# Performance work log

Hardware: AMD Instinct MI355X
Metric: run time of the kernel (lower is better)

Reference implementation:

```python
import jax, jax.numpy as jnp
import numpy as np
import math

D_MODEL = 1024
EPS = 1e-6  # RMSNorm epsilon


def setup_inputs() -> dict:
    key = jax.random.key(0)
    ks = jax.random.split(key, 9)
    d = D_MODEL
    B, T = 4, 4096
    s = 1.0 / math.sqrt(d)
    return {
        "x": jax.random.normal(ks[0], (B, T, d), dtype=jnp.float32),
        "w_key": jax.random.normal(ks[1], (2 * d, d), dtype=jnp.float32) * s,  # Linear(d, 2d, bias=False)
        "conv_w": jax.random.normal(ks[2], (d, 1, 3), dtype=jnp.float32) * (1.0 / math.sqrt(3)),  # depthwise k=3
        "conv_b": jax.random.normal(ks[3], (d,), dtype=jnp.float32) * 0.02,
        "w1": jax.random.normal(ks[4], (2 * d, d), dtype=jnp.float32) * s,  # Linear(d, 2d)
        "b1": jax.random.normal(ks[5], (2 * d,), dtype=jnp.float32) * 0.02,
        "w2": jax.random.normal(ks[6], (d, 2 * d), dtype=jnp.float32) * (1.0 / math.sqrt(2 * d)),  # Linear(2d, d)
        "b2": jax.random.normal(ks[7], (d,), dtype=jnp.float32) * 0.02,
        "norm_w": jnp.ones((d,), dtype=jnp.float32),
    }


def parallel_lerp_scan(theta, alpha):
    # h_t = lerp(h_{t-1}, theta_t, alpha_t) = (1-alpha_t)*h_{t-1} + alpha_t*theta_t
    # Linear recurrence h_t = a_t*h_{t-1} + b_t -> log-depth associative scan.
    a = 1.0 - alpha
    b = alpha * theta

    def combine(c1, c2):
        a1, b1 = c1
        a2, b2 = c2
        return (a2 * a1, a2 * b1 + b2)

    _, h = jax.lax.associative_scan(combine, (a, b), axis=1)
    return h


def rms_norm(x, w):
    var = jnp.mean(jnp.square(x), axis=-1, keepdims=True)
    return x * jax.lax.rsqrt(var + EPS) * w


def reference(x, w_key, conv_w, conv_b, w1, b1, w2, b2, norm_w):
    d = x.shape[-1]
    res = jnp.einsum('btd,ed->bte', x, w_key)  # [B,T,2D]
    theta, alpha = res[..., :d], res[..., d:]
    h = parallel_lerp_scan(jnp.tanh(theta) * math.pi, jax.nn.sigmoid(alpha))
    h = h.astype(x.dtype)
    # causal depthwise conv: left-pad (k-1)=2 zeros along time
    h_t = jnp.transpose(h, (0, 2, 1))  # [B,D,T]
    conv = jax.lax.conv_general_dilated(
        h_t, conv_w, window_strides=(1,), padding=[(2, 0)],
        feature_group_count=d, dimension_numbers=('NCH', 'OIH', 'NCH'))
    h_bound = jnp.transpose(conv + conv_b[None, :, None], (0, 2, 1))  # [B,T,D]
    z = h + h_bound
    hid = jax.nn.silu(jnp.einsum('btd,ed->bte', z, w1) + b1)
    h_final = jnp.einsum('bte,de->btd', hid, w2) + b2
    return rms_norm(h_final, norm_w)
```

## Files before the change

### kernel.cpp

```cpp
#include <hip/hip_runtime.h>

typedef unsigned short u16;
typedef unsigned int u32;
typedef __attribute__((ext_vector_type(8))) short short8;
typedef __attribute__((ext_vector_type(4))) float f32x4;

#define T_LEN 4096
#define BATCH 4
#define M_TOT (BATCH*T_LEN)
#define NCHUNK 64
#define CLEN 64

__device__ __forceinline__ u16 f2bf(float f){
  u32 u = __builtin_bit_cast(u32, f);
  u32 r = (u + 0x7FFFu + ((u >> 16) & 1u)) >> 16;
  return (u16)r;
}
__device__ __forceinline__ float bf2f(u16 h){
  u32 u = ((u32)h) << 16; return __builtin_bit_cast(float, u);
}
__device__ __forceinline__ float sigmoid_(float v){ return 1.f/(1.f + __expf(-v)); }
__device__ __forceinline__ float tanh_pi_(float v){
  return 3.14159265358979323846f * (1.f - 2.f/(1.f + __expf(2.f*v)));
}

__global__ __launch_bounds__(256) void cvt_bf16_k(const float* __restrict__ in,
                                                  u16* __restrict__ out, int n4){
  int g = blockIdx.x*256 + threadIdx.x;
  if (g >= n4) return;
  float4 v = reinterpret_cast<const float4*>(in)[g];
  reinterpret_cast<ushort4*>(out)[g] =
      make_ushort4(f2bf(v.x), f2bf(v.y), f2bf(v.z), f2bf(v.w));
}

#define BAR() __builtin_amdgcn_s_barrier()
#define VMCNT(n) asm volatile("s_waitcnt vmcnt(" #n ")" ::: "memory")
#define LGKM0() asm volatile("s_waitcnt lgkmcnt(0)" ::: "memory")
#define LGKM8() asm volatile("s_waitcnt lgkmcnt(8)" ::: "memory")
#define FEN() asm volatile("" ::: "memory")
#define PRIO1() __builtin_amdgcn_s_setprio(1)
#define PRIO0() __builtin_amdgcn_s_setprio(0)

#define STAGE(buf, ab, q, kt) do { \
  const u16* _s = ((ab) ? Bb : Ab) + (size_t)(q)*rowK64 + (size_t)(kt)*64; \
  __builtin_amdgcn_global_load_lds( \
    (const __attribute__((address_space(1))) void*)_s, \
    (__attribute__((address_space(3))) void*)(smem + (buf)*65536 + (ab)*32768 + (q)*8192 + stb), \
    16, 0, 0); \
} while(0)

#define LDA(base, m, kk) (*(const short8*)((base) + (m)*2048 + ((kk) ? csw1 : csw0)))
#define LDB(base, n, kk) (*(const short8*)((base) + (n)*2048 + ((kk) ? csw1 : csw0)))

#define RD_A(base, h) do { _Pragma("unroll") \
  for (int ml=0; ml<4; ml++){ \
    aF[ml*2+0] = LDA(base, 4*(h)+ml, 0); \
    aF[ml*2+1] = LDA(base, 4*(h)+ml, 1); } } while(0)

#define RD_B(base, h) do { _Pragma("unroll") \
  for (int nl=0; nl<2; nl++){ \
    bF[(h)*4+nl*2+0] = LDB(base, 2*(h)+nl, 0); \
    bF[(h)*4+nl*2+1] = LDB(base, 2*(h)+nl, 1); } } while(0)

#define MFMAQ(mh, nh) do { _Pragma("unroll") \
  for (int kk=0; kk<2; kk++) \
  _Pragma("unroll") \
  for (int ml=0; ml<4; ml++) \
  _Pragma("unroll") \
  for (int nl=0; nl<2; nl++) \
    acc[4*(mh)+ml][2*(nh)+nl] = __builtin_amdgcn_mfma_f32_16x16x32_bf16( \
      aF[ml*2+kk], bF[(nh)*4+nl*2+kk], acc[4*(mh)+ml][2*(nh)+nl], 0,0,0); \
} while(0)

template<int EPI>
__global__ __launch_bounds__(512, 2) void gemm8p(
    const u16* __restrict__ Ag, const u16* __restrict__ Bg,
    const float* __restrict__ bias, void* __restrict__ Cout,
    int M, int N, int K)
{
  extern __shared__ __attribute__((aligned(16))) char smem[];
  const int tid = threadIdx.x;
  const int wid = tid >> 6, lane = tid & 63;
  const int wr = wid >> 2, wc = wid & 3;
  const int fr = lane & 15, fq = lane >> 4;

  const int nbn = N >> 8;
  const int nwg = gridDim.x;
  const int bid = blockIdx.x;
  const int swzb = (bid & 7) * (nwg >> 3) + (bid >> 3);
  const int bm = swzb / nbn, bn = swzb - bm * nbn;

  const size_t rowK64 = (size_t)64 * K;
  const u16* Ab = Ag + ((size_t)bm*256 + (tid>>3)) * K + ((tid & 7) ^ ((tid >> 3) & 7)) * 8;
  const u16* Bb = Bg + ((size_t)bn*256 + (tid>>3)) * K + ((tid & 7) ^ ((tid >> 3) & 7)) * 8;
  const u32 stb = (u32)(wid << 10);

  const u32 csw0 = (u32)((fq*16)      ^ ((fr & 7) << 4));
  const u32 csw1 = (u32)((64 + fq*16) ^ ((fr & 7) << 4));
  const char* aB0 = smem +         (u32)(wr*128 + fr) * 128;
  const char* aB1 = aB0 + 65536;
  const char* bB0 = smem + 32768 + (u32)(wc*64  + fr) * 128;
  const char* bB1 = bB0 + 65536;

  f32x4 acc[8][4];
#pragma unroll
  for (int m=0;m<8;m++)
#pragma unroll
    for (int n=0;n<4;n++) acc[m][n] = f32x4{0.f,0.f,0.f,0.f};

  short8 aF[8];
  short8 bF[8];

  const int NT = K >> 6;

  STAGE(0,0,0,0); STAGE(0,0,1,0); STAGE(0,0,2,0); STAGE(0,0,3,0);
  STAGE(0,1,0,0); STAGE(0,1,1,0); STAGE(0,1,2,0); STAGE(0,1,3,0);
  STAGE(1,0,0,1); STAGE(1,0,2,1);
  STAGE(1,1,0,1); STAGE(1,1,1,1); STAGE(1,1,2,1); STAGE(1,1,3,1);
  VMCNT(6);
  BAR();

  for (int i = 0; i < (NT>>1) - 1; ++i){
    const int tt = 2*i;
    RD_A(aB0,0); RD_B(bB0,0); FEN();
    STAGE(1,0,1,tt+1); STAGE(1,0,3,tt+1);
    LGKM8();
    BAR(); LGKM0();
    PRIO1(); MFMAQ(0,0); PRIO0();
    BAR();
    RD_B(bB0,1); FEN();
    STAGE(0,0,0,tt+2); STAGE(0,0,2,tt+2);
    BAR(); LGKM0();
    PRIO1(); MFMAQ(0,1); PRIO0();
    BAR();
    RD_A(aB0,1); FEN();
    STAGE(0,1,0,tt+2); STAGE(0,1,1,tt+2);
    BAR(); LGKM0();
    PRIO1(); MFMAQ(1,0); PRIO0();
    BAR();
    STAGE(0,1,2,tt+2); STAGE(0,1,3,tt+2);
    BAR();
    PRIO1(); MFMAQ(1,1); PRIO0();
    VMCNT(6);
    BAR();
    RD_A(aB1,0); RD_B(bB1,0); FEN();
    STAGE(0,0,1,tt+2); STAGE(0,0,3,tt+2);
    LGKM8();
    BAR(); LGKM0();
    PRIO1(); MFMAQ(0,0); PRIO0();
    BAR();
    RD_B(bB1,1); FEN();
    STAGE(1,0,0,tt+3); STAGE(1,0,2,tt+3);
    BAR(); LGKM0();
    PRIO1(); MFMAQ(0,1); PRIO0();
    BAR();
    RD_A(aB1,1); FEN();
    STAGE(1,1,0,tt+3); STAGE(1,1,1,tt+3);
    BAR(); LGKM0();
    PRIO1(); MFMAQ(1,0); PRIO0();
    BAR();
    STAGE(1,1,2,tt+3); STAGE(1,1,3,tt+3);
    BAR();
    PRIO1(); MFMAQ(1,1); PRIO0();
    VMCNT(6);
    BAR();
  }
  {
    RD_A(aB0,0); RD_B(bB0,0); FEN();
    STAGE(1,0,1,NT-1); STAGE(1,0,3,NT-1);
    LGKM8();
    BAR(); LGKM0();
    PRIO1(); MFMAQ(0,0); PRIO0();
    BAR();
    RD_B(bB0,1); FEN();
    BAR(); LGKM0();
    PRIO1(); MFMAQ(0,1); PRIO0();
    BAR();
    RD_A(aB0,1); FEN();
    BAR(); LGKM0();
    PRIO1(); MFMAQ(1,0); PRIO0();
    BAR();
    BAR();
    PRIO1(); MFMAQ(1,1); PRIO0();
    VMCNT(0);
    BAR();
    RD_A(aB1,0); RD_B(bB1,0); FEN();
    BAR(); LGKM0();
    PRIO1(); MFMAQ(0,0); PRIO0();
    BAR();
    RD_B(bB1,1); FEN();
    BAR(); LGKM0();
    PRIO1(); MFMAQ(0,1); PRIO0();
    BAR();
    RD_A(aB1,1); FEN();
    BAR(); LGKM0();
    PRIO1(); MFMAQ(1,0); PRIO0();
    BAR();
    PRIO1(); MFMAQ(1,1); PRIO0();
  }

  const int orow0 = bm*256 + wr*128;
  const int ocol0 = bn*256 + wc*64;
#pragma unroll
  for (int m=0;m<8;m++){
#pragma unroll
    for (int n=0;n<4;n++){
      const int col = ocol0 + n*16 + fr;
#pragma unroll
      for (int r=0;r<4;r++){
        const int row = orow0 + m*16 + fq*4 + r;
        float v = acc[m][n][r];
        if constexpr (EPI == 0){
          float o = (col < 1024) ? tanh_pi_(v) : sigmoid_(v);
          ((u16*)Cout)[(size_t)row*N + col] = f2bf(o);
        } else if constexpr (EPI == 1){
          v += bias[col];
          ((u16*)Cout)[(size_t)row*N + col] = f2bf(v * sigmoid_(v));
        } else {
          v += bias[col];
          ((float*)Cout)[(size_t)row*N + col] = v;
        }
      }
    }
  }
}

__global__ __launch_bounds__(256) void scan_stage1(const u16* __restrict__ res,
                                                   float* __restrict__ sA,
                                                   float* __restrict__ sB,
                                                   float* __restrict__ sA2,
                                                   float* __restrict__ sB2){
  const int c0    = ((blockIdx.x & 1)*256 + threadIdx.x)*2;
  const int chunk = (blockIdx.x >> 1) & (NCHUNK-1);
  const int b     = blockIdx.x >> 7;
  const u16* p = res + ((size_t)(b*T_LEN + chunk*CLEN))*2048 + c0;
  float A0=1.f, B0v=0.f, A1=1.f, B1v=0.f;
#pragma unroll 4
  for (int t=0;t<CLEN-1;++t){
    ushort2 th = *reinterpret_cast<const ushort2*>(p);
    ushort2 sg = *reinterpret_cast<const ushort2*>(p+1024);
    float s0 = bf2f(sg.x), s1 = bf2f(sg.y);
    float a0 = 1.f - s0,   a1 = 1.f - s1;
    A0 *= a0;  B0v = a0*B0v + s0*bf2f(th.x);
    A1 *= a1;  B1v = a1*B1v + s1*bf2f(th.y);
    p += 2048;
  }
  const int idx = (b*NCHUNK + chunk)*1024 + c0;
  *reinterpret_cast<float2*>(&sA2[idx]) = make_float2(A0, A1);
  *reinterpret_cast<float2*>(&sB2[idx]) = make_float2(B0v, B1v);
  {
    ushort2 th = *reinterpret_cast<const ushort2*>(p);
    ushort2 sg = *reinterpret_cast<const ushort2*>(p+1024);
    float s0 = bf2f(sg.x), s1 = bf2f(sg.y);
    float a0 = 1.f - s0,   a1 = 1.f - s1;
    A0 *= a0;  B0v = a0*B0v + s0*bf2f(th.x);
    A1 *= a1;  B1v = a1*B1v + s1*bf2f(th.y);
  }
  *reinterpret_cast<float2*>(&sA[idx]) = make_float2(A0, A1);
  *reinterpret_cast<float2*>(&sB[idx]) = make_float2(B0v, B1v);
}

__global__ __launch_bounds__(256) void scan_stage2(const float* __restrict__ sA,
                                                   const float* __restrict__ sB,
                                                   float* __restrict__ Hp){
  const int g = blockIdx.x*256 + threadIdx.x;
  const int b = g >> 10, c = g & 1023;
  float H = 0.f;
#pragma unroll
  for (int i=0;i<NCHUNK;++i){
    const int idx = (b*NCHUNK + i)*1024 + c;
    Hp[idx] = H;
    H = sA[idx]*H + sB[idx];
  }
}

__global__ __launch_bounds__(256) void scan3_conv_k(const u16* __restrict__ res,
                                                    const float* __restrict__ Hp,
                                                    const float* __restrict__ sA2,
                                                    const float* __restrict__ sB2,
                                                    const float* __restrict__ cw,
                                                    const float* __restrict__ cb,
                                                    u16* __restrict__ z){
  const int c0    = ((blockIdx.x & 1)*256 + threadIdx.x)*2;
  const int chunk = (blockIdx.x >> 1) & (NCHUNK-1);
  const int b     = blockIdx.x >> 7;
  const u16* p = res + ((size_t)(b*T_LEN + chunk*CLEN))*2048 + c0;
  u16*       q = z   + ((size_t)(b*T_LEN + chunk*CLEN))*1024 + c0;
  const int idx = (b*NCHUNK + chunk)*1024 + c0;
  float H0 = Hp[idx], H1 = Hp[idx+1];
  float hm1_0 = H0, hm1_1 = H1;
  float hm2_0 = 0.f, hm2_1 = 0.f;
  if (chunk > 0){
    const int pidx = idx - 1024;
    hm2_0 = sA2[pidx]*Hp[pidx] + sB2[pidx];
    hm2_1 = sA2[pidx+1]*Hp[pidx+1] + sB2[pidx+1];
  }
  const float w0_0 = cw[3*c0],   w1_0 = cw[3*c0+1], w2_0 = cw[3*c0+2], bb0 = cb[c0];
  const float w0_1 = cw[3*c0+3], w1_1 = cw[3*c0+4], w2_1 = cw[3*c0+5], bb1 = cb[c0+1];
#pragma unroll 4
  for (int t=0;t<CLEN;++t){
    ushort2 th = *reinterpret_cast<const ushort2*>(p);
    ushort2 sg = *reinterpret_cast<const ushort2*>(p+1024);
    float s0 = bf2f(sg.x), s1 = bf2f(sg.y);
    H0 = (1.f - s0)*H0 + s0*bf2f(th.x);
    H1 = (1.f - s1)*H1 + s1*bf2f(th.y);
    float v0 = H0 + bb0 + hm2_0*w0_0 + hm1_0*w1_0 + H0*w2_0;
    float v1 = H1 + bb1 + hm2_1*w0_1 + hm1_1*w1_1 + H1*w2_1;
    *reinterpret_cast<ushort2*>(q) = make_ushort2(f2bf(v0), f2bf(v1));
    hm2_0 = hm1_0; hm1_0 = H0;
    hm2_1 = hm1_1; hm1_1 = H1;
    p += 2048; q += 1024;
  }
}

__global__ __launch_bounds__(256) void rmsnorm_k(float* __restrict__ io,
                                                 const float* __restrict__ w){
  const int row = blockIdx.x;
  const int tid = threadIdx.x;
  float* p = io + (size_t)row*1024;
  float4 v = reinterpret_cast<const float4*>(p)[tid];
  float ss = v.x*v.x + v.y*v.y + v.z*v.z + v.w*v.w;
#pragma unroll
  for (int o=32; o>0; o>>=1) ss += __shfl_xor(ss, o, 64);
  __shared__ float red[4];
  if ((tid & 63) == 0) red[tid >> 6] = ss;
  __syncthreads();
  float tot = red[0] + red[1] + red[2] + red[3];
  float scale = rsqrtf(tot * (1.f/1024.f) + 1e-6f);
  float4 wv = reinterpret_cast<const float4*>(w)[tid];
  float4 o;
  o.x = v.x*scale*wv.x; o.y = v.y*scale*wv.y;
  o.z = v.z*scale*wv.z; o.w = v.w*scale*wv.w;
  reinterpret_cast<float4*>(p)[tid] = o;
}

extern "C" void kernel_launch(void* const* d_in, const int* in_sizes, int n_in,
                              void* d_out, int out_size, void* d_ws, size_t ws_size,
                              hipStream_t stream) {
  const float* x      = (const float*)d_in[0];
  const float* w_key  = (const float*)d_in[1];
  const float* conv_w = (const float*)d_in[2];
  const float* conv_b = (const float*)d_in[3];
  const float* w1     = (const float*)d_in[4];
  const float* b1     = (const float*)d_in[5];
  const float* w2     = (const float*)d_in[6];
  const float* b2     = (const float*)d_in[7];
  const float* norm_w = (const float*)d_in[8];
  float* out = (float*)d_out;
  char*  ws  = (char*)d_ws;

  size_t off = 0;
  u16*   RES  = (u16*)  (ws + off); off += (size_t)M_TOT*2048*2;
  u16*   XB   = (u16*)  (ws + off); off += (size_t)M_TOT*1024*2;
  u16*   WK   = (u16*)  (ws + off); off += (size_t)2048*1024*2;
  u16*   W1B  = (u16*)  (ws + off); off += (size_t)2048*1024*2;
  u16*   W2B  = (u16*)  (ws + off); off += (size_t)1024*2048*2;
  float* SA   = (float*)(ws + off); off += (size_t)BATCH*NCHUNK*1024*4;
  float* SB   = (float*)(ws + off); off += (size_t)BATCH*NCHUNK*1024*4;
  float* SA2  = (float*)(ws + off); off += (size_t)BATCH*NCHUNK*1024*4;
  float* SB2  = (float*)(ws + off); off += (size_t)BATCH*NCHUNK*1024*4;
  float* HP   = (float*)(ws + off); off += (size_t)BATCH*NCHUNK*1024*4;
  u16* ZB  = XB;
  u16* HID = RES;

  hipFuncSetAttribute((const void*)gemm8p<0>, hipFuncAttributeMaxDynamicSharedMemorySize, 131072);
  hipFuncSetAttribute((const void*)gemm8p<1>, hipFuncAttributeMaxDynamicSharedMemorySize, 131072);
  hipFuncSetAttribute((const void*)gemm8p<2>, hipFuncAttributeMaxDynamicSharedMemorySize, 131072);

  cvt_bf16_k<<<(M_TOT*1024/4 + 255)/256, 256, 0, stream>>>(x,     XB,  M_TOT*1024/4);
  cvt_bf16_k<<<(2048*1024/4  + 255)/256, 256, 0, stream>>>(w_key, WK,  2048*1024/4);
  cvt_bf16_k<<<(2048*1024/4  + 255)/256, 256, 0, stream>>>(w1,    W1B, 2048*1024/4);
  cvt_bf16_k<<<(1024*2048/4  + 255)/256, 256, 0, stream>>>(w2,    W2B, 1024*2048/4);

  gemm8p<0><<<(M_TOT/256)*(2048/256), 512, 131072, stream>>>(XB, WK, nullptr, RES, M_TOT, 2048, 1024);

  scan_stage1<<<BATCH*NCHUNK*2, 256, 0, stream>>>(RES, SA, SB, SA2, SB2);
  scan_stage2<<<16, 256, 0, stream>>>(SA, SB, HP);
  scan3_conv_k<<<BATCH*NCHUNK*2, 256, 0, stream>>>(RES, HP, SA2, SB2, conv_w, conv_b, ZB);

  gemm8p<1><<<(M_TOT/256)*(2048/256), 512, 131072, stream>>>(ZB, W1B, b1, HID, M_TOT, 2048, 1024);

  gemm8p<2><<<(M_TOT/256)*(1024/256), 512, 131072, stream>>>(HID, W2B, b2, out, M_TOT, 1024, 2048);

  rmsnorm_k<<<M_TOT, 256, 0, stream>>>(out, norm_w);
}
```

Baseline: 308.3 us.

## Shrink GEMM tile to 128x256 with 4 waves and K-step 32

Reworks the bf16 MFMA GEMM from a 256x256 tile with 8 waves and 64-wide K steps to a 128x256 tile with 4 waves and 32-wide K steps. Shared memory drops from 128KB to 48KB per block, and the swizzled LDS layout and fragment reads are redone to match. The aim is more resident blocks per CU and a larger grid for better load balance. The cost is lower arithmetic intensity per block, more global traffic for the weight operand, and twice as many barrier-heavy K iterations.

```diff
diff --git a/kernel.cpp b/kernel.cpp
--- a/kernel.cpp
+++ b/kernel.cpp
@@ -36,44 +36,36 @@
 #define BAR() __builtin_amdgcn_s_barrier()
 #define VMCNT(n) asm volatile("s_waitcnt vmcnt(" #n ")" ::: "memory")
 #define LGKM0() asm volatile("s_waitcnt lgkmcnt(0)" ::: "memory")
-#define LGKM8() asm volatile("s_waitcnt lgkmcnt(8)" ::: "memory")
 #define FEN() asm volatile("" ::: "memory")
 #define PRIO1() __builtin_amdgcn_s_setprio(1)
 #define PRIO0() __builtin_amdgcn_s_setprio(0)
 
 #define STAGE(buf, ab, q, kt) do { \
-  const u16* _s = ((ab) ? Bb : Ab) + (size_t)(q)*rowK64 + (size_t)(kt)*64; \
+  const u16* _s = ((ab) ? Bb : Ab) + (size_t)(q)*64*K + (size_t)(kt)*32; \
   __builtin_amdgcn_global_load_lds( \
     (const __attribute__((address_space(1))) void*)_s, \
-    (__attribute__((address_space(3))) void*)(smem + (buf)*65536 + (ab)*32768 + (q)*8192 + stb), \
+    (__attribute__((address_space(3))) void*)(smem + (buf)*24576 + (ab)*8192 + (q)*4096 + stb), \
     16, 0, 0); \
 } while(0)
 
-#define LDA(base, m, kk) (*(const short8*)((base) + (m)*2048 + ((kk) ? csw1 : csw0)))
-#define LDB(base, n, kk) (*(const short8*)((base) + (n)*2048 + ((kk) ? csw1 : csw0)))
-
 #define RD_A(base, h) do { _Pragma("unroll") \
-  for (int ml=0; ml<4; ml++){ \
-    aF[ml*2+0] = LDA(base, 4*(h)+ml, 0); \
-    aF[ml*2+1] = LDA(base, 4*(h)+ml, 1); } } while(0)
+  for (int ml=0; ml<2; ml++) \
+    aF[ml] = *(const short8*)((base) + ((h)*2+ml)*1024); } while(0)
 
 #define RD_B(base, h) do { _Pragma("unroll") \
-  for (int nl=0; nl<2; nl++){ \
-    bF[(h)*4+nl*2+0] = LDB(base, 2*(h)+nl, 0); \
-    bF[(h)*4+nl*2+1] = LDB(base, 2*(h)+nl, 1); } } while(0)
+  for (int nl=0; nl<4; nl++) \
+    bF[(h)*4+nl] = *(const short8*)((base) + ((h)*4+nl)*1024); } while(0)
 
 #define MFMAQ(mh, nh) do { _Pragma("unroll") \
-  for (int kk=0; kk<2; kk++) \
+  for (int ml=0; ml<2; ml++) \
   _Pragma("unroll") \
-  for (int ml=0; ml<4; ml++) \
-  _Pragma("unroll") \
-  for (int nl=0; nl<2; nl++) \
-    acc[4*(mh)+ml][2*(nh)+nl] = __builtin_amdgcn_mfma_f32_16x16x32_bf16( \
-      aF[ml*2+kk], bF[(nh)*4+nl*2+kk], acc[4*(mh)+ml][2*(nh)+nl], 0,0,0); \
+  for (int nl=0; nl<4; nl++) \
+    acc[2*(mh)+ml][4*(nh)+nl] = __builtin_amdgcn_mfma_f32_16x16x32_bf16( \
+      aF[ml], bF[4*(nh)+nl], acc[2*(mh)+ml][4*(nh)+nl], 0,0,0); \
 } while(0)
 
 template<int EPI>
-__global__ __launch_bounds__(512, 2) void gemm8p(
+__global__ __launch_bounds__(256, 2) void gemm8p(
     const u16* __restrict__ Ag, const u16* __restrict__ Bg,
     const float* __restrict__ bias, void* __restrict__ Cout,
     int M, int N, int K)
@@ -81,7 +73,7 @@
   extern __shared__ __attribute__((aligned(16))) char smem[];
   const int tid = threadIdx.x;
   const int wid = tid >> 6, lane = tid & 63;
-  const int wr = wid >> 2, wc = wid & 3;
+  const int wr = wid >> 1, wc = wid & 1;
   const int fr = lane & 15, fq = lane >> 4;
 
   const int nbn = N >> 8;
@@ -90,76 +82,72 @@
   const int swzb = (bid & 7) * (nwg >> 3) + (bid >> 3);
   const int bm = swzb / nbn, bn = swzb - bm * nbn;
 
-  const size_t rowK64 = (size_t)64 * K;
-  const u16* Ab = Ag + ((size_t)bm*256 + (tid>>3)) * K + ((tid & 7) ^ ((tid >> 3) & 7)) * 8;
-  const u16* Bb = Bg + ((size_t)bn*256 + (tid>>3)) * K + ((tid & 7) ^ ((tid >> 3) & 7)) * 8;
+  const u32 uu = (u32)((tid & 7) ^ ((tid >> 3) & 7));
+  const u16* Ab = Ag + ((size_t)bm*128 + 2*(tid>>3) + (uu>>2))*K + (uu&3)*8;
+  const u16* Bb = Bg + ((size_t)bn*256 + 2*(tid>>3) + (uu>>2))*K + (uu&3)*8;
   const u32 stb = (u32)(wid << 10);
 
-  const u32 csw0 = (u32)((fq*16)      ^ ((fr & 7) << 4));
-  const u32 csw1 = (u32)((64 + fq*16) ^ ((fr & 7) << 4));
-  const char* aB0 = smem +         (u32)(wr*128 + fr) * 128;
-  const char* aB1 = aB0 + 65536;
-  const char* bB0 = smem + 32768 + (u32)(wc*64  + fr) * 128;
-  const char* bB1 = bB0 + 65536;
-
-  f32x4 acc[8][4];
-#pragma unroll
-  for (int m=0;m<8;m++)
-#pragma unroll
-    for (int n=0;n<4;n++) acc[m][n] = f32x4{0.f,0.f,0.f,0.f};
-
-  short8 aF[8];
+  const u32 csw = (u32)((((fr&1)*64) + fq*16) ^ (((fr>>1)&7) << 4));
+  const char* aB0 = smem +        (u32)(wr*32 + (fr>>1))*128 + csw;
+  const char* bB0 = smem + 8192 + (u32)(wc*64 + (fr>>1))*128 + csw;
+  const char* aB1 = aB0 + 24576;
+  const char* bB1 = bB0 + 24576;
+
+  f32x4 acc[4][8];
+#pragma unroll
+  for (int m=0;m<4;m++)
+#pragma unroll
+    for (int n=0;n<8;n++) acc[m][n] = f32x4{0.f,0.f,0.f,0.f};
+
+  short8 aF[2];
   short8 bF[8];
 
-  const int NT = K >> 6;
-
-  STAGE(0,0,0,0); STAGE(0,0,1,0); STAGE(0,0,2,0); STAGE(0,0,3,0);
+  const int NT = K >> 5;
+  const int NPAIR = NT >> 1;
+
+  STAGE(0,0,0,0); STAGE(0,0,1,0);
   STAGE(0,1,0,0); STAGE(0,1,1,0); STAGE(0,1,2,0); STAGE(0,1,3,0);
-  STAGE(1,0,0,1); STAGE(1,0,2,1);
+  STAGE(1,0,0,1); STAGE(1,0,1,1);
   STAGE(1,1,0,1); STAGE(1,1,1,1); STAGE(1,1,2,1); STAGE(1,1,3,1);
   VMCNT(6);
   BAR();
 
-  for (int i = 0; i < (NT>>1) - 1; ++i){
+  for (int i = 0; i < NPAIR - 1; ++i){
     const int tt = 2*i;
     RD_A(aB0,0); RD_B(bB0,0); FEN();
-    STAGE(1,0,1,tt+1); STAGE(1,0,3,tt+1);
-    LGKM8();
     BAR(); LGKM0();
     PRIO1(); MFMAQ(0,0); PRIO0();
     BAR();
     RD_B(bB0,1); FEN();
-    STAGE(0,0,0,tt+2); STAGE(0,0,2,tt+2);
+    STAGE(0,1,0,tt+2); STAGE(0,1,2,tt+2);
     BAR(); LGKM0();
     PRIO1(); MFMAQ(0,1); PRIO0();
     BAR();
     RD_A(aB0,1); FEN();
-    STAGE(0,1,0,tt+2); STAGE(0,1,1,tt+2);
+    STAGE(0,1,1,tt+2); STAGE(0,1,3,tt+2);
     BAR(); LGKM0();
     PRIO1(); MFMAQ(1,0); PRIO0();
     BAR();
-    STAGE(0,1,2,tt+2); STAGE(0,1,3,tt+2);
+    STAGE(0,0,0,tt+2); STAGE(0,0,1,tt+2);
     BAR();
     PRIO1(); MFMAQ(1,1); PRIO0();
     VMCNT(6);
     BAR();
     RD_A(aB1,0); RD_B(bB1,0); FEN();
-    STAGE(0,0,1,tt+2); STAGE(0,0,3,tt+2);
-    LGKM8();
     BAR(); LGKM0();
     PRIO1(); MFMAQ(0,0); PRIO0();
     BAR();
     RD_B(bB1,1); FEN();
-    STAGE(1,0,0,tt+3); STAGE(1,0,2,tt+3);
+    STAGE(1,1,0,tt+3); STAGE(1,1,2,tt+3);
     BAR(); LGKM0();
     PRIO1(); MFMAQ(0,1); PRIO0();
     BAR();
     RD_A(aB1,1); FEN();
-    STAGE(1,1,0,tt+3); STAGE(1,1,1,tt+3);
+    STAGE(1,1,1,tt+3); STAGE(1,1,3,tt+3);
     BAR(); LGKM0();
     PRIO1(); MFMAQ(1,0); PRIO0();
     BAR();
-    STAGE(1,1,2,tt+3); STAGE(1,1,3,tt+3);
+    STAGE(1,0,0,tt+3); STAGE(1,0,1,tt+3);
     BAR();
     PRIO1(); MFMAQ(1,1); PRIO0();
     VMCNT(6);
@@ -167,8 +155,6 @@
   }
   {
     RD_A(aB0,0); RD_B(bB0,0); FEN();
-    STAGE(1,0,1,NT-1); STAGE(1,0,3,NT-1);
-    LGKM8();
     BAR(); LGKM0();
     PRIO1(); MFMAQ(0,0); PRIO0();
     BAR();
@@ -199,12 +185,12 @@
     PRIO1(); MFMAQ(1,1); PRIO0();
   }
 
-  const int orow0 = bm*256 + wr*128;
-  const int ocol0 = bn*256 + wc*64;
-#pragma unroll
-  for (int m=0;m<8;m++){
-#pragma unroll
-    for (int n=0;n<4;n++){
+  const int orow0 = bm*128 + wr*64;
+  const int ocol0 = bn*256 + wc*128;
+#pragma unroll
+  for (int m=0;m<4;m++){
+#pragma unroll
+    for (int n=0;n<8;n++){
       const int col = ocol0 + n*16 + fr;
 #pragma unroll
       for (int r=0;r<4;r++){
@@ -363,24 +349,24 @@
   u16* ZB  = XB;
   u16* HID = RES;
 
-  hipFuncSetAttribute((const void*)gemm8p<0>, hipFuncAttributeMaxDynamicSharedMemorySize, 131072);
-  hipFuncSetAttribute((const void*)gemm8p<1>, hipFuncAttributeMaxDynamicSharedMemorySize, 131072);
-  hipFuncSetAttribute((const void*)gemm8p<2>, hipFuncAttributeMaxDynamicSharedMemorySize, 131072);
+  hipFuncSetAttribute((const void*)gemm8p<0>, hipFuncAttributeMaxDynamicSharedMemorySize, 49152);
+  hipFuncSetAttribute((const void*)gemm8p<1>, hipFuncAttributeMaxDynamicSharedMemorySize, 49152);
+  hipFuncSetAttribute((const void*)gemm8p<2>, hipFuncAttributeMaxDynamicSharedMemorySize, 49152);
 
   cvt_bf16_k<<<(M_TOT*1024/4 + 255)/256, 256, 0, stream>>>(x,     XB,  M_TOT*1024/4);
   cvt_bf16_k<<<(2048*1024/4  + 255)/256, 256, 0, stream>>>(w_key, WK,  2048*1024/4);
   cvt_bf16_k<<<(2048*1024/4  + 255)/256, 256, 0, stream>>>(w1,    W1B, 2048*1024/4);
   cvt_bf16_k<<<(1024*2048/4  + 255)/256, 256, 0, stream>>>(w2,    W2B, 1024*2048/4);
 
-  gemm8p<0><<<(M_TOT/256)*(2048/256), 512, 131072, stream>>>(XB, WK, nullptr, RES, M_TOT, 2048, 1024);
+  gemm8p<0><<<(M_TOT/128)*(2048/256), 256, 49152, stream>>>(XB, WK, nullptr, RES, M_TOT, 2048, 1024);
 
   scan_stage1<<<BATCH*NCHUNK*2, 256, 0, stream>>>(RES, SA, SB, SA2, SB2);
   scan_stage2<<<16, 256, 0, stream>>>(SA, SB, HP);
   scan3_conv_k<<<BATCH*NCHUNK*2, 256, 0, stream>>>(RES, HP, SA2, SB2, conv_w, conv_b, ZB);
 
-  gemm8p<1><<<(M_TOT/256)*(2048/256), 512, 131072, stream>>>(ZB, W1B, b1, HID, M_TOT, 2048, 1024);
-
-  gemm8p<2><<<(M_TOT/256)*(1024/256), 512, 131072, stream>>>(HID, W2B, b2, out, M_TOT, 1024, 2048);
+  gemm8p<1><<<(M_TOT/128)*(2048/256), 256, 49152, stream>>>(ZB, W1B, b1, HID, M_TOT, 2048, 1024);
+
+  gemm8p<2><<<(M_TOT/128)*(1024/256), 256, 49152, stream>>>(HID, W2B, b2, out, M_TOT, 1024, 2048);
 
   rmsnorm_k<<<M_TOT, 256, 0, stream>>>(out, norm_w);
 }
```

Result: slower. 330.0 us (+7.0%).
